# Kernel tuning notes

Measured on AMD Instinct MI355X. Metric: run time of the kernel, lower is better.

The kernel has to match this reference:

```python
import jax, jax.numpy as jnp
import numpy as np

# ---------- static mesh topology helpers (numpy, setup-time only) ----------

def _topo_subdivide(nv, faces):
    edge_id = {}
    mids = []
    nf = []
    def mid(a, b):
        k = (a, b) if a < b else (b, a)
        if k not in edge_id:
            edge_id[k] = nv + len(mids)
            mids.append(k)
        return edge_id[k]
    for a, b, c in faces:
        a, b, c = int(a), int(b), int(c)
        ab, bc, ca = mid(a, b), mid(b, c), mid(c, a)
        nf += [[a, ab, ca], [b, bc, ab], [c, ca, bc], [ab, bc, ca]]
    return np.array(nf, dtype=np.int64), np.array(mids, dtype=np.int64)

def _icosphere(level, radius):
    t = (1.0 + 5.0 ** 0.5) / 2.0
    v = np.array([[-1, t, 0], [1, t, 0], [-1, -t, 0], [1, -t, 0],
                  [0, -1, t], [0, 1, t], [0, -1, -t], [0, 1, -t],
                  [t, 0, -1], [t, 0, 1], [-t, 0, -1], [-t, 0, 1]], dtype=np.float64)
    v /= np.linalg.norm(v, axis=1, keepdims=True)
    f = np.array([[0, 11, 5], [0, 5, 1], [0, 1, 7], [0, 7, 10], [0, 10, 11],
                  [1, 5, 9], [5, 11, 4], [11, 10, 2], [10, 7, 6], [7, 1, 8],
                  [3, 9, 4], [3, 4, 2], [3, 2, 6], [3, 6, 8], [3, 8, 9],
                  [4, 9, 5], [2, 4, 11], [6, 2, 10], [8, 6, 7], [9, 8, 1]], dtype=np.int64)
    for _ in range(level):
        f, mids = _topo_subdivide(len(v), f)
        mv = v[mids[:, 0]] + v[mids[:, 1]]
        mv /= np.linalg.norm(mv, axis=1, keepdims=True)
        v = np.concatenate([v, mv], 0)
    return (v * radius).astype(np.float32), f

def _directed_edges(faces):
    e = np.concatenate([faces[:, [0, 1]], faces[:, [1, 2]], faces[:, [2, 0]],
                        faces[:, [1, 0]], faces[:, [2, 1]], faces[:, [0, 2]]], 0)
    return np.unique(e, axis=0).T.astype(np.int64)  # (2, E) directed, deduped

# ---------- jax forward math ----------

def _project(verts, camera_c, camera_f):
    # K @ [I | t], t = (0,0,0.8): rows [f0,0,c0,0.8*c0],[0,f1,c1,0.8*c1],[0,0,1,0.8]
    z = jnp.zeros((), verts.dtype); o = jnp.ones((), verts.dtype)
    tz = jnp.asarray(0.8, verts.dtype)
    P = jnp.stack([
        jnp.stack([camera_f[0], z, camera_c[0], tz * camera_c[0]]),
        jnp.stack([z, camera_f[1], camera_c[1], tz * camera_c[1]]),
        jnp.stack([z, z, o, tz])])
    hom = jnp.concatenate([verts, jnp.ones((verts.shape[0], 1), verts.dtype)], 1)
    pc = hom @ P.T                     # (V, 3)
    return pc[:, :2] / pc[:, 2:3]      # (V, 2) pixel coords [x, y]

def _bilerp(feat, px, py, image_size):
    # feat: (C, dim, dim); px, py: (V,)
    dim = feat.shape[1]
    x = px * dim / image_size
    y = py * dim / image_size
    x1 = jnp.floor(x); x2 = x1 + 1.0
    y1 = jnp.floor(y); y2 = y1 + 1.0
    xi1 = jnp.clip(x1.astype(jnp.int32), 0, dim - 1)
    xi2 = jnp.clip(x2.astype(jnp.int32), 0, dim - 1)
    yi1 = jnp.clip(y1.astype(jnp.int32), 0, dim - 1)
    yi2 = jnp.clip(y2.astype(jnp.int32), 0, dim - 1)
    f11 = feat[:, xi1, yi1].T  # (V, C)
    f12 = feat[:, xi1, yi2].T
    f21 = feat[:, xi2, yi1].T
    f22 = feat[:, xi2, yi2].T
    w11 = ((x2 - x) * (y2 - y))[:, None]
    w12 = ((x2 - x) * (y - y1))[:, None]
    w21 = ((x - x1) * (y2 - y))[:, None]
    w22 = ((x - x1) * (y - y1))[:, None]
    return w11 * f11 + w12 * f12 + w21 * f21 + w22 * f22

def _gconv(x, W0, W1, b, src, dst):
    agg = jax.ops.segment_sum(x[dst], src, num_segments=x.shape[0])
    return x @ W0 + agg @ W1 + b

def _gresnet(x, edges, params):
    Win0, Win1, bin_, W0s, W1s, bs, Wc0, Wc1, bc = params
    src, dst = edges[0], edges[1]
    h = jax.nn.relu(_gconv(x, Win0, Win1, bin_, src, dst))
    def body(h, lw):
        W0, W1, b = lw
        return jax.nn.relu(_gconv(h, W0, W1, b, src, dst)) + h, None
    h, _ = jax.lax.scan(body, h, (W0s, W1s, bs))
    coords = _gconv(h, Wc0, Wc1, bc, src, dst)
    return h, coords

def _forward(f3, f4, f5, verts0, camera_c, camera_f, p1, p2, p3,
             edges1, edges2, edges3, mid0, mid1, image_size):
    def deform(verts, shape_feat, edges, params):
        pix = _project(verts, camera_c, camera_f)
        px, py = pix[:, 0], pix[:, 1]
        perc = jnp.concatenate([_bilerp(f3, px, py, image_size),
                                _bilerp(f4, px, py, image_size),
                                _bilerp(f5, px, py, image_size)], 1)  # (V, 1280)
        feats = jnp.concatenate([perc, shape_feat], 1)
        h, coords = _gresnet(feats, edges, params)
        return coords, h
    def unpool(verts, feat, mid):
        vf = jnp.concatenate([verts, feat], 1)
        new = (vf[mid[:, 0]] + vf[mid[:, 1]]) * 0.5  # edge midpoints
        vf = jnp.concatenate([vf, new], 0)
        return vf[:, :3], vf[:, 3:]
    verts, feat = deform(verts0, verts0, edges1, p1)
    verts, feat = unpool(verts, feat, mid0)
    verts, feat = deform(verts, feat, edges2, p2)
    verts, feat = unpool(verts, feat, mid1)
    verts, _ = deform(verts, feat, edges3, p3)
    return verts  # (40962, 3)

# ---------- harness entry points ----------

def setup_inputs() -> dict:
    key = jax.random.key(0)
    keys = iter(jax.random.split(key, 64))
    v0, f0 = _icosphere(4, 0.2)                      # 2562 verts, 5120 faces
    f1, mid0 = _topo_subdivide(len(v0), f0)          # -> 10242 verts topology
    f2, mid1 = _topo_subdivide(len(v0) + len(mid0), f1)  # -> 40962 verts
    inp = {
        'f3': jax.random.normal(next(keys), (256, 56, 56), jnp.float32),
        'f4': jax.random.normal(next(keys), (512, 28, 28), jnp.float32),
        'f5': jax.random.normal(next(keys), (512, 14, 14), jnp.float32),
        'verts0': jnp.asarray(v0),
        'camera_c': jnp.array([112.0, 112.0], jnp.float32),
        'camera_f': jnp.array([248.0, 248.0], jnp.float32),
    }
    D, L = 128, 12
    def stage(prefix, in_dim):
        def w(shape, scale):
            return jax.random.normal(next(keys), shape, jnp.float32) * scale
        inp[prefix + '_Win0'] = w((in_dim, D), 1.0 / np.sqrt(in_dim))
        inp[prefix + '_Win1'] = w((in_dim, D), 1.0 / np.sqrt(in_dim))
        inp[prefix + '_bin'] = jnp.zeros((D,), jnp.float32)
        inp[prefix + '_W0'] = w((L, D, D), 0.3 / np.sqrt(D))
        inp[prefix + '_W1'] = w((L, D, D), 0.3 / np.sqrt(D))
        inp[prefix + '_b'] = jnp.zeros((L, D), jnp.float32)
        inp[prefix + '_Wc0'] = w((D, 3), 0.01 / np.sqrt(D))
        inp[prefix + '_Wc1'] = w((D, 3), 0.01 / np.sqrt(D))
        inp[prefix + '_bc'] = jnp.zeros((3,), jnp.float32)
    stage('g1', 1283)
    stage('g2', 1408)
    stage('g3', 1408)
    inp['edges1'] = jnp.asarray(_directed_edges(f0))   # (2, 15360)
    inp['edges2'] = jnp.asarray(_directed_edges(f1))   # (2, 61440)
    inp['edges3'] = jnp.asarray(_directed_edges(f2))   # (2, 245760)
    inp['mid0'] = jnp.asarray(mid0)                    # (7680, 2)
    inp['mid1'] = jnp.asarray(mid1)                    # (30720, 2)
    inp['image_size'] = 224
    return inp

def reference(f3, f4, f5, verts0, camera_c, camera_f,
              g1_Win0, g1_Win1, g1_bin, g1_W0, g1_W1, g1_b, g1_Wc0, g1_Wc1, g1_bc,
              g2_Win0, g2_Win1, g2_bin, g2_W0, g2_W1, g2_b, g2_Wc0, g2_Wc1, g2_bc,
              g3_Win0, g3_Win1, g3_bin, g3_W0, g3_W1, g3_b, g3_Wc0, g3_Wc1, g3_bc,
              edges1, edges2, edges3, mid0, mid1, image_size):
    p1 = (g1_Win0, g1_Win1, g1_bin, g1_W0, g1_W1, g1_b, g1_Wc0, g1_Wc1, g1_bc)
    p2 = (g2_Win0, g2_Win1, g2_bin, g2_W0, g2_W1, g2_b, g2_Wc0, g2_Wc1, g2_bc)
    p3 = (g3_Win0, g3_Win1, g3_bin, g3_W0, g3_W1, g3_b, g3_Wc0, g3_Wc1, g3_bc)
    return _forward(f3, f4, f5, verts0, camera_c, camera_f, p1, p2, p3,
                    edges1, edges2, edges3, mid0, mid1, image_size)
```

## Files before the change

### kernel.cpp

```cpp
#include <hip/hip_runtime.h>
#include <hip/hip_bf16.h>
#include <cstddef>
#include <cstdint>

#define DIV_UP(a, b) (((a) + (b) - 1) / (b))

typedef __attribute__((ext_vector_type(8))) short bf16x8v;
typedef __attribute__((ext_vector_type(4))) float f32x4v;

__device__ __forceinline__ unsigned short bf16_rn(float v) {
    unsigned int u = __float_as_uint(v);
    unsigned int r = (u + 0x7FFFu + ((u >> 16) & 1u)) >> 16;
    return (unsigned short)r;
}
__device__ __forceinline__ float bf16_f(unsigned short h) {
    return __uint_as_float(((unsigned int)h) << 16);
}
__device__ __forceinline__ void f2hl(float v, unsigned short& hi, unsigned short& lo) {
    hi = bf16_rn(v);
    float r = v - bf16_f(hi);
    lo = bf16_rn(r);
}
__device__ __forceinline__ int xcd_swz(int orig, int nwg) {
    int q = nwg >> 3, r = nwg & 7;
    int xcd = orig & 7, idx = orig >> 3;
    return (xcd < r ? xcd * (q + 1) : r * (q + 1) + (xcd - r) * q) + idx;
}

__global__ void transpose_hl(const float* __restrict__ in, unsigned short* __restrict__ ohi,
                             unsigned short* __restrict__ olo, int C, int HW) {
    int idx = blockIdx.x * 256 + threadIdx.x;
    if (idx >= C * HW) return;
    int c = idx % C;
    int p = idx / C;
    float v = in[(size_t)c * HW + p];
    unsigned short hi, lo;
    f2hl(v, hi, lo);
    ohi[(size_t)p * C + c] = hi;
    olo[(size_t)p * C + c] = lo;
}

struct PackArgs {
    const float* Win0[3]; const float* Win1[3];
    const float* W0L[3];  const float* W1L[3];
    unsigned short* BtLp[3];
    unsigned short *BtShi[2], *BtSlo[2];
    unsigned short *Bgh[3], *Bgl[3];
};

__global__ void pack_all(PackArgs p) {
    const int LAY1 = 12 * 32768;
    const int LAYT = 3 * LAY1;
    const int SH1 = 256 * 128;
    const int SHT = 2 * SH1;
    const int GB0 = 768 * 256, GB1 = 768 * 512;
    int idx = blockIdx.x * 256 + threadIdx.x;
    if (idx < LAYT) {
        int st = idx / LAY1, r = idx % LAY1;
        int layer = r >> 15, q = r & 32767;
        int ks = q >> 12, nt = (q >> 9) & 7, lane = (q >> 3) & 63, i = q & 7;
        int n = nt * 16 + (lane & 15);
        int k = ks * 32 + ((lane >> 4) << 3) + i;
        float v = (k < 128) ? p.W0L[st][(size_t)layer * 16384 + k * 128 + n]
                            : p.W1L[st][(size_t)layer * 16384 + (k - 128) * 128 + n];
        unsigned short hi, lo;
        f2hl(v, hi, lo);
        size_t base = ((size_t)layer * 64 + ks * 8 + nt) * 1024 + lane * 8 + i;
        p.BtLp[st][base] = hi;
        p.BtLp[st][base + 512] = lo;
        return;
    }
    float v;
    unsigned short* dh;
    unsigned short* dl;
    size_t o;
    if (idx < LAYT + SHT) {
        int q = idx - LAYT;
        int st = q / SH1, rr = q % SH1;
        int n = rr >> 7, k = rr & 127;
        const float* w0 = p.Win0[st + 1];
        const float* w1 = p.Win1[st + 1];
        v = (n < 128) ? w0[(size_t)(1280 + k) * 128 + n]
                      : w1[(size_t)(1280 + k) * 128 + (n - 128)];
        dh = p.BtShi[st]; dl = p.BtSlo[st]; o = rr;
    } else {
        int q = idx - LAYT - SHT;
        int m, C, base;
        if (q < GB0) { m = 0; C = 256; base = 0; }
        else if (q < GB0 + GB1) { m = 1; C = 512; base = 256; q -= GB0; }
        else if (q < GB0 + 2 * GB1) { m = 2; C = 512; base = 768; q -= GB0 + GB1; }
        else return;
        int n = q / C, k = q % C;
        int s = n >> 8, j = n & 255;
        v = (j < 128) ? p.Win0[s][(size_t)(base + k) * 128 + j]
                      : p.Win1[s][(size_t)(base + k) * 128 + (j - 128)];
        dh = p.Bgh[m]; dl = p.Bgl[m]; o = q;
    }
    unsigned short hi, lo;
    f2hl(v, hi, lo);
    dh[o] = hi;
    dl[o] = lo;
}

__global__ void desc_adj_kernel(const float* __restrict__ verts,
                                const float* __restrict__ cam_c, const float* __restrict__ cam_f,
                                const int* __restrict__ imgsz, int V,
                                const int* __restrict__ src, const int* __restrict__ dst, int E,
                                int* __restrict__ sampi, float* __restrict__ sampw,
                                int* __restrict__ adj8) {
    int v = blockIdx.x * 256 + threadIdx.x;
    if (v >= V) return;
    float X = verts[3 * v + 0], Yy = verts[3 * v + 1], Z = verts[3 * v + 2];
    float cx = cam_c[0], cy = cam_c[1], fx = cam_f[0], fy = cam_f[1];
    const float tz = 0.8f;
    float pz = Z + tz;
    float px = (fx * X + cx * Z + tz * cx) / pz;
    float py = (fy * Yy + cy * Z + tz * cy) / pz;
    float is = (float)imgsz[0];
    const int Ss[3] = {56, 28, 14};
#pragma unroll
    for (int m = 0; m < 3; ++m) {
        int S = Ss[m];
        float dim = (float)S;
        float x = px * dim / is;
        float y = py * dim / is;
        float x1 = floorf(x), y1 = floorf(y);
        float x2 = x1 + 1.0f, y2 = y1 + 1.0f;
        float smax = (float)(S - 1);
        int xi1 = (int)fminf(fmaxf(x1, 0.0f), smax);
        int xi2 = (int)fminf(fmaxf(x2, 0.0f), smax);
        int yi1 = (int)fminf(fmaxf(y1, 0.0f), smax);
        int yi2 = (int)fminf(fmaxf(y2, 0.0f), smax);
        int b = v * 12 + m * 4;
        sampi[b + 0] = xi1 * S + yi1;
        sampi[b + 1] = xi1 * S + yi2;
        sampi[b + 2] = xi2 * S + yi1;
        sampi[b + 3] = xi2 * S + yi2;
        sampw[b + 0] = (x2 - x) * (y2 - y);
        sampw[b + 1] = (x2 - x) * (y - y1);
        sampw[b + 2] = (x - x1) * (y2 - y);
        sampw[b + 3] = (x - x1) * (y - y1);
    }
    int lo = 0, hi = E;
    while (lo < hi) { int m = (lo + hi) >> 1; if (src[m] < v) lo = m + 1; else hi = m; }
    int e0 = lo;
    hi = E;
    while (lo < hi) { int m = (lo + hi) >> 1; if (src[m] < v + 1) lo = m + 1; else hi = m; }
    int e1 = lo;
    int* ap = adj8 + (size_t)v * 8;
#pragma unroll
    for (int i = 0; i < 8; ++i) {
        int e = e0 + i;
        ap[i] = (e < e1) ? dst[e] : -1;
    }
}

struct MArgs {
    const unsigned short *Ahi, *Alo; int lda;
    const unsigned short *Bhi, *Blo; int K;
    float* Y;
    int sstr;
    int V;
};

template <int EPI>
__global__ __launch_bounds__(256) void mgemm(MArgs g) {
    __shared__ unsigned short As_hi[64][40], As_lo[64][40];
    __shared__ unsigned short Bs_hi[128][40], Bs_lo[128][40];
    int tid = threadIdx.x;
    int row0 = blockIdx.y * 64;
    int col0 = blockIdx.x * 128;
    int l = tid & 63, wid = tid >> 6;
    int wr = wid & 1, wc = wid >> 1;
    int lw = l & 15, gg = l >> 4;
    f32x4v acc[2][4];
#pragma unroll
    for (int i = 0; i < 2; ++i)
#pragma unroll
        for (int j = 0; j < 4; ++j) acc[i][j] = (f32x4v){0.f, 0.f, 0.f, 0.f};

    int arow = tid >> 2, akoff = (tid & 3) * 8;
    for (int k0 = 0; k0 < g.K; k0 += 32) {
        __syncthreads();
        {
            int grow = row0 + arow;
            uint4 zh = make_uint4(0, 0, 0, 0), zl = make_uint4(0, 0, 0, 0);
            if (grow < g.V) {
                zh = *(const uint4*)(g.Ahi + (size_t)grow * g.lda + k0 + akoff);
                zl = *(const uint4*)(g.Alo + (size_t)grow * g.lda + k0 + akoff);
            }
            *(uint4*)&As_hi[arow][akoff] = zh;
            *(uint4*)&As_lo[arow][akoff] = zl;
        }
#pragma unroll
        for (int it = 0; it < 2; ++it) {
            int q = tid + it * 256;
            int n = q >> 2, koff = (q & 3) * 8;
            *(uint4*)&Bs_hi[n][koff] = *(const uint4*)(g.Bhi + (size_t)(col0 + n) * g.K + k0 + koff);
            *(uint4*)&Bs_lo[n][koff] = *(const uint4*)(g.Blo + (size_t)(col0 + n) * g.K + k0 + koff);
        }
        __syncthreads();
        bf16x8v ah[2], al[2], bh[4], bl[4];
#pragma unroll
        for (int mt = 0; mt < 2; ++mt) {
            int r = wr * 32 + mt * 16 + lw;
            ah[mt] = *(const bf16x8v*)&As_hi[r][gg * 8];
            al[mt] = *(const bf16x8v*)&As_lo[r][gg * 8];
        }
#pragma unroll
        for (int nt = 0; nt < 4; ++nt) {
            int c = wc * 64 + nt * 16 + lw;
            bh[nt] = *(const bf16x8v*)&Bs_hi[c][gg * 8];
            bl[nt] = *(const bf16x8v*)&Bs_lo[c][gg * 8];
        }
#pragma unroll
        for (int mt = 0; mt < 2; ++mt)
#pragma unroll
            for (int nt = 0; nt < 4; ++nt) {
                acc[mt][nt] = __builtin_amdgcn_mfma_f32_16x16x32_bf16(ah[mt], bh[nt], acc[mt][nt], 0, 0, 0);
                acc[mt][nt] = __builtin_amdgcn_mfma_f32_16x16x32_bf16(ah[mt], bl[nt], acc[mt][nt], 0, 0, 0);
                acc[mt][nt] = __builtin_amdgcn_mfma_f32_16x16x32_bf16(al[mt], bh[nt], acc[mt][nt], 0, 0, 0);
            }
    }
#pragma unroll
    for (int mt = 0; mt < 2; ++mt)
#pragma unroll
        for (int nt = 0; nt < 4; ++nt) {
            int colg = wc * 64 + nt * 16 + lw;
#pragma unroll
            for (int r = 0; r < 4; ++r) {
                int rowg = row0 + wr * 32 + mt * 16 + gg * 4 + r;
                if (rowg >= g.V) continue;
                float v = acc[mt][nt][r];
                if (EPI == 3) {
                    g.Y[(size_t)rowg * 256 + col0 + colg] = v;
                } else {
                    int cg = col0 + colg;
                    g.Y[(size_t)(cg >> 8) * g.sstr + (size_t)rowg * 256 + (cg & 255)] = v;
                }
            }
        }
}

__global__ void gather_kernel(const float* __restrict__ G, int sstr,
                              const int* __restrict__ sampi, const float* __restrict__ sampw,
                              float* __restrict__ Yb, int V, int stage,
                              const float* __restrict__ Win0, const float* __restrict__ Win1,
                              const float* __restrict__ shape) {
    int v = xcd_swz(blockIdx.x, gridDim.x) * 4 + (threadIdx.x >> 6);
    if (v >= V) return;
    int j = (threadIdx.x & 63) * 4;
    const float* Gs = G + (size_t)stage * sstr;
    int b = v * 12;
    float4 acc;
    if (stage == 0) acc = make_float4(0.f, 0.f, 0.f, 0.f);
    else acc = *(const float4*)(Yb + (size_t)v * 256 + j);
#pragma unroll
    for (int s = 0; s < 4; ++s) {
        float w = sampw[b + s];
        float4 f = *(const float4*)(Gs + (size_t)sampi[b + s] * 256 + j);
        acc.x += w * f.x; acc.y += w * f.y; acc.z += w * f.z; acc.w += w * f.w;
    }
#pragma unroll
    for (int s = 0; s < 4; ++s) {
        float w = sampw[b + 4 + s];
        float4 f = *(const float4*)(Gs + (size_t)(3136 + sampi[b + 4 + s]) * 256 + j);
        acc.x += w * f.x; acc.y += w * f.y; acc.z += w * f.z; acc.w += w * f.w;
    }
#pragma unroll
    for (int s = 0; s < 4; ++s) {
        float w = sampw[b + 8 + s];
        float4 f = *(const float4*)(Gs + (size_t)(3920 + sampi[b + 8 + s]) * 256 + j);
        acc.x += w * f.x; acc.y += w * f.y; acc.z += w * f.z; acc.w += w * f.w;
    }
    if (stage == 0) {
#pragma unroll
        for (int k = 0; k < 3; ++k) {
            float w = shape[v * 3 + k];
            const float* wr = (j < 128) ? Win0 + (size_t)(1280 + k) * 128 + j
                                        : Win1 + (size_t)(1280 + k) * 128 + (j - 128);
            float4 wv = *(const float4*)wr;
            acc.x += w * wv.x; acc.y += w * wv.y; acc.z += w * wv.z; acc.w += w * wv.w;
        }
    }
    *(float4*)(Yb + (size_t)v * 256 + j) = acc;
}

__global__ __launch_bounds__(256) void combine_in(
    const float* __restrict__ Y, const float* __restrict__ bias,
    const int* __restrict__ adj8,
    float* __restrict__ hout, int V) {
    int v = xcd_swz(blockIdx.x, gridDim.x) * 8 + (threadIdx.x >> 5);
    if (v >= V) return;
    int d = (threadIdx.x & 31) * 4;
    float4 val = *(const float4*)(Y + (size_t)v * 256 + d);
    float4 b4 = *(const float4*)(bias + d);
    val.x += b4.x; val.y += b4.y; val.z += b4.z; val.w += b4.w;
    const int* ap = adj8 + (size_t)v * 8;
    int n[6];
#pragma unroll
    for (int i = 0; i < 6; ++i) n[i] = ap[i];
#pragma unroll
    for (int i = 0; i < 6; ++i) {
        if (n[i] >= 0) {
            float4 f = *(const float4*)(Y + (size_t)n[i] * 256 + 128 + d);
            val.x += f.x; val.y += f.y; val.z += f.z; val.w += f.w;
        }
    }
    val.x = fmaxf(val.x, 0.f); val.y = fmaxf(val.y, 0.f);
    val.z = fmaxf(val.z, 0.f); val.w = fmaxf(val.w, 0.f);
    *(float4*)(hout + (size_t)v * 128 + d) = val;
}

struct LArgs {
    const float* h;
    const unsigned short* Bp;
    const int* adj8;
    const float* bias;
    float* hnext;
    int V;
};

template <int PAIRS>
__global__ __launch_bounds__(PAIRS * 128) void lay_kernel(LArgs g) {
    __shared__ float psum[PAIRS][16][132];
    int tid = threadIdx.x;
    int wid = tid >> 6, l = tid & 63;
    int pair = wid >> 1, role = wid & 1;
    int rowbase = xcd_swz(blockIdx.x, gridDim.x) * (PAIRS * 16) + pair * 16;
    int lrow = l & 15, lks = l >> 4;
    int grow = rowbase + lrow;
    bool act = grow < g.V;

    f32x4v acc[8];
#pragma unroll
    for (int nt = 0; nt < 8; ++nt) acc[nt] = (f32x4v){0.f, 0.f, 0.f, 0.f};

    if (role == 0) {
        const float* hp = g.h + (size_t)grow * 128;
#pragma unroll
        for (int ks = 0; ks < 4; ++ks) {
            int kb = ks * 32 + lks * 8;
            float a[8];
            if (act) {
                float4 f0 = *(const float4*)(hp + kb);
                float4 f1 = *(const float4*)(hp + kb + 4);
                a[0] = f0.x; a[1] = f0.y; a[2] = f0.z; a[3] = f0.w;
                a[4] = f1.x; a[5] = f1.y; a[6] = f1.z; a[7] = f1.w;
            } else {
#pragma unroll
                for (int i = 0; i < 8; ++i) a[i] = 0.f;
            }
            unsigned short hh[8], ll[8];
#pragma unroll
            for (int i = 0; i < 8; ++i) f2hl(a[i], hh[i], ll[i]);
            bf16x8v ah = *(const bf16x8v*)hh;
            bf16x8v al = *(const bf16x8v*)ll;
#pragma unroll
            for (int nt = 0; nt < 8; ++nt) {
                const unsigned short* p = g.Bp + (size_t)(ks * 8 + nt) * 1024 + l * 8;
                bf16x8v bh = *(const bf16x8v*)p;
                bf16x8v bl = *(const bf16x8v*)(p + 512);
                acc[nt] = __builtin_amdgcn_mfma_f32_16x16x32_bf16(ah, bh, acc[nt], 0, 0, 0);
                acc[nt] = __builtin_amdgcn_mfma_f32_16x16x32_bf16(ah, bl, acc[nt], 0, 0, 0);
                acc[nt] = __builtin_amdgcn_mfma_f32_16x16x32_bf16(al, bh, acc[nt], 0, 0, 0);
            }
        }
    } else {
        int n[6];
        if (act) {
            const int* ap = g.adj8 + (size_t)grow * 8;
#pragma unroll
            for (int i = 0; i < 6; ++i) n[i] = ap[i];
        } else {
#pragma unroll
            for (int i = 0; i < 6; ++i) n[i] = -1;
        }
#pragma unroll
        for (int ks = 0; ks < 4; ++ks) {
            int ko = ks * 32 + lks * 8;
            float a[8];
#pragma unroll
            for (int i = 0; i < 8; ++i) a[i] = 0.f;
#pragma unroll
            for (int i = 0; i < 6; ++i) {
                if (n[i] >= 0) {
                    const float* hp = g.h + (size_t)n[i] * 128 + ko;
                    float4 f0 = *(const float4*)hp;
                    float4 f1 = *(const float4*)(hp + 4);
                    a[0] += f0.x; a[1] += f0.y; a[2] += f0.z; a[3] += f0.w;
                    a[4] += f1.x; a[5] += f1.y; a[6] += f1.z; a[7] += f1.w;
                }
            }
            unsigned short hh[8], ll[8];
#pragma unroll
            for (int i = 0; i < 8; ++i) f2hl(a[i], hh[i], ll[i]);
            bf16x8v ah = *(const bf16x8v*)hh;
            bf16x8v al = *(const bf16x8v*)ll;
#pragma unroll
            for (int nt = 0; nt < 8; ++nt) {
                const unsigned short* p = g.Bp + (size_t)((ks + 4) * 8 + nt) * 1024 + l * 8;
                bf16x8v bh = *(const bf16x8v*)p;
                bf16x8v bl = *(const bf16x8v*)(p + 512);
                acc[nt] = __builtin_amdgcn_mfma_f32_16x16x32_bf16(ah, bh, acc[nt], 0, 0, 0);
                acc[nt] = __builtin_amdgcn_mfma_f32_16x16x32_bf16(ah, bl, acc[nt], 0, 0, 0);
                acc[nt] = __builtin_amdgcn_mfma_f32_16x16x32_bf16(al, bh, acc[nt], 0, 0, 0);
            }
        }
#pragma unroll
        for (int nt = 0; nt < 8; ++nt)
#pragma unroll
            for (int r = 0; r < 4; ++r)
                psum[pair][lks * 4 + r][nt * 16 + lrow] = acc[nt][r];
    }
    __syncthreads();
    if (role == 0) {
#pragma unroll
        for (int nt = 0; nt < 8; ++nt) {
            int colg = nt * 16 + lrow;
            float bv = g.bias[colg];
#pragma unroll
            for (int r = 0; r < 4; ++r) {
                int rowg = rowbase + lks * 4 + r;
                if (rowg < g.V) {
                    float v = acc[nt][r] + psum[pair][lks * 4 + r][colg] + bv;
                    v = fmaxf(v, 0.0f);
                    v += g.h[(size_t)rowg * 128 + colg];
                    g.hnext[(size_t)rowg * 128 + colg] = v;
                }
            }
        }
    }
}

__global__ void coordgemm_kernel(const float* __restrict__ h,
                                 const float* __restrict__ Wc0, const float* __restrict__ Wc1,
                                 int V, float* __restrict__ Yc) {
    int idx = blockIdx.x * 256 + threadIdx.x;
    if (idx >= V * 6) return;
    int v = idx / 6, j = idx % 6;
    const float* W = (j < 3) ? Wc0 : Wc1;
    int jj = (j < 3) ? j : j - 3;
    const float* hp = h + (size_t)v * 128;
    float acc = 0.0f;
#pragma unroll
    for (int k = 0; k < 32; ++k) {
        float4 f = *(const float4*)(hp + k * 4);
        acc += f.x * W[(k * 4 + 0) * 3 + jj];
        acc += f.y * W[(k * 4 + 1) * 3 + jj];
        acc += f.z * W[(k * 4 + 2) * 3 + jj];
        acc += f.w * W[(k * 4 + 3) * 3 + jj];
    }
    Yc[idx] = acc;
}

__global__ void coordcombine_kernel(const float* __restrict__ Yc, const float* __restrict__ bc,
                                    const int* __restrict__ adj8,
                                    int V, float* __restrict__ out) {
    int idx = blockIdx.x * 256 + threadIdx.x;
    if (idx >= V * 3) return;
    int v = idx / 3, j = idx % 3;
    float val = Yc[(size_t)v * 6 + j] + bc[j];
    const int* ap = adj8 + (size_t)v * 8;
    int n[6];
#pragma unroll
    for (int i = 0; i < 6; ++i) n[i] = ap[i];
#pragma unroll
    for (int i = 0; i < 6; ++i)
        if (n[i] >= 0) val += Yc[(size_t)n[i] * 6 + 3 + j];
    out[(size_t)v * 3 + j] = val;
}

__global__ void unpool_kernel(float* __restrict__ verts, const float* __restrict__ h,
                              const int* __restrict__ mid, int V, int Nm,
                              unsigned short* __restrict__ fphi, unsigned short* __restrict__ fplo) {
    int r = blockIdx.x;
    int t = threadIdx.x;
    if (r < V) {
        float v = h[(size_t)r * 128 + t];
        unsigned short hi, lo;
        f2hl(v, hi, lo);
        fphi[(size_t)r * 128 + t] = hi;
        fplo[(size_t)r * 128 + t] = lo;
    } else {
        int i = r - V;
        int a = mid[2 * i], b = mid[2 * i + 1];
        float v = 0.5f * (h[(size_t)a * 128 + t] + h[(size_t)b * 128 + t]);
        unsigned short hi, lo;
        f2hl(v, hi, lo);
        fphi[(size_t)r * 128 + t] = hi;
        fplo[(size_t)r * 128 + t] = lo;
        if (t < 3)
            verts[(size_t)r * 3 + t] = 0.5f * (verts[(size_t)a * 3 + t] + verts[(size_t)b * 3 + t]);
    }
}

extern "C" void kernel_launch(void* const* d_in, const int* in_sizes, int n_in,
                              void* d_out, int out_size, void* d_ws, size_t ws_size,
                              hipStream_t stream) {
    const float* f3 = (const float*)d_in[0];
    const float* f4 = (const float*)d_in[1];
    const float* f5 = (const float*)d_in[2];
    const float* verts0 = (const float*)d_in[3];
    const float* cam_c = (const float*)d_in[4];
    const float* cam_f = (const float*)d_in[5];
    const int* imgsz = (const int*)d_in[38];

    int V0 = in_sizes[3] / 3;
    int E[3] = {in_sizes[33] / 2, in_sizes[34] / 2, in_sizes[35] / 2};
    int Nm0 = in_sizes[36] / 2, Nm1 = in_sizes[37] / 2;
    int V1 = V0 + Nm0, V2 = V1 + Nm1;
    int Vs[3] = {V0, V1, V2};
    const int NPIXT = 3136 + 784 + 196;
    const int GS = NPIXT * 256;

    char* wsp = (char*)d_ws;
    auto alloc = [&](size_t bytes) -> void* {
        void* p = (void*)wsp;
        wsp += (bytes + 255) & ~(size_t)255;
        return p;
    };
    unsigned short* ft0h = (unsigned short*)alloc((size_t)3136 * 256 * 2);
    unsigned short* ft0l = (unsigned short*)alloc((size_t)3136 * 256 * 2);
    unsigned short* ft1h = (unsigned short*)alloc((size_t)784 * 512 * 2);
    unsigned short* ft1l = (unsigned short*)alloc((size_t)784 * 512 * 2);
    unsigned short* ft2h = (unsigned short*)alloc((size_t)196 * 512 * 2);
    unsigned short* ft2l = (unsigned short*)alloc((size_t)196 * 512 * 2);
    unsigned short* Bg0h = (unsigned short*)alloc((size_t)768 * 256 * 2);
    unsigned short* Bg0l = (unsigned short*)alloc((size_t)768 * 256 * 2);
    unsigned short* Bg1h = (unsigned short*)alloc((size_t)768 * 512 * 2);
    unsigned short* Bg1l = (unsigned short*)alloc((size_t)768 * 512 * 2);
    unsigned short* Bg2h = (unsigned short*)alloc((size_t)768 * 512 * 2);
    unsigned short* Bg2l = (unsigned short*)alloc((size_t)768 * 512 * 2);
    float* Gbuf = (float*)alloc((size_t)3 * GS * 4);
    unsigned short* BtLp[3];
    for (int s = 0; s < 3; ++s)
        BtLp[s] = (unsigned short*)alloc((size_t)12 * 65536 * 2);
    unsigned short* BtShi[2];
    unsigned short* BtSlo[2];
    for (int s = 0; s < 2; ++s) {
        BtShi[s] = (unsigned short*)alloc((size_t)256 * 128 * 2);
        BtSlo[s] = (unsigned short*)alloc((size_t)256 * 128 * 2);
    }
    float* Ybuf = (float*)alloc((size_t)V2 * 256 * 4);
    float* hA = (float*)alloc((size_t)V2 * 128 * 4);
    float* hB = (float*)alloc((size_t)V2 * 128 * 4);
    unsigned short* FPhi = (unsigned short*)alloc((size_t)V2 * 128 * 2);
    unsigned short* FPlo = (unsigned short*)alloc((size_t)V2 * 128 * 2);
    float* vertsbuf = (float*)alloc((size_t)V2 * 3 * 4);
    float* Yc = (float*)alloc((size_t)V2 * 6 * 4);
    int* sampi = (int*)alloc((size_t)V2 * 12 * 4);
    float* sampw = (float*)alloc((size_t)V2 * 12 * 4);
    int* adj8 = (int*)alloc((size_t)V2 * 8 * 4);

    transpose_hl<<<DIV_UP(256 * 56 * 56, 256), 256, 0, stream>>>(f3, ft0h, ft0l, 256, 56 * 56);
    transpose_hl<<<DIV_UP(512 * 28 * 28, 256), 256, 0, stream>>>(f4, ft1h, ft1l, 512, 28 * 28);
    transpose_hl<<<DIV_UP(512 * 14 * 14, 256), 256, 0, stream>>>(f5, ft2h, ft2l, 512, 14 * 14);

    {
        PackArgs p;
        for (int s = 0; s < 3; ++s) {
            p.Win0[s] = (const float*)d_in[6 + s * 9 + 0];
            p.Win1[s] = (const float*)d_in[6 + s * 9 + 1];
            p.W0L[s] = (const float*)d_in[6 + s * 9 + 3];
            p.W1L[s] = (const float*)d_in[6 + s * 9 + 4];
            p.BtLp[s] = BtLp[s];
        }
        p.BtShi[0] = BtShi[0]; p.BtSlo[0] = BtSlo[0];
        p.BtShi[1] = BtShi[1]; p.BtSlo[1] = BtSlo[1];
        p.Bgh[0] = Bg0h; p.Bgl[0] = Bg0l;
        p.Bgh[1] = Bg1h; p.Bgl[1] = Bg1l;
        p.Bgh[2] = Bg2h; p.Bgl[2] = Bg2l;
        int total = 3 * 12 * 32768 + 2 * 256 * 128 + 768 * 256 + 2 * 768 * 512;
        pack_all<<<DIV_UP(total, 256), 256, 0, stream>>>(p);
    }

    {
        MArgs m = {};
        m.sstr = GS;
        m.Ahi = ft0h; m.Alo = ft0l; m.lda = 256;
        m.Bhi = Bg0h; m.Blo = Bg0l; m.K = 256;
        m.Y = Gbuf; m.V = 3136;
        dim3 g0(6, DIV_UP(3136, 64));
        mgemm<2><<<g0, 256, 0, stream>>>(m);
        m.Ahi = ft1h; m.Alo = ft1l; m.lda = 512;
        m.Bhi = Bg1h; m.Blo = Bg1l; m.K = 512;
        m.Y = Gbuf + (size_t)3136 * 256; m.V = 784;
        dim3 g1(6, DIV_UP(784, 64));
        mgemm<2><<<g1, 256, 0, stream>>>(m);
        m.Ahi = ft2h; m.Alo = ft2l; m.lda = 512;
        m.Bhi = Bg2h; m.Blo = Bg2l; m.K = 512;
        m.Y = Gbuf + (size_t)3920 * 256; m.V = 196;
        dim3 g2(6, DIV_UP(196, 64));
        mgemm<2><<<g2, 256, 0, stream>>>(m);
    }

    for (int si = 0; si < 3; ++si) {
        const float* Win0 = (const float*)d_in[6 + si * 9 + 0];
        const float* Win1 = (const float*)d_in[6 + si * 9 + 1];
        const float* bin = (const float*)d_in[6 + si * 9 + 2];
        const float* bs = (const float*)d_in[6 + si * 9 + 5];
        const float* Wc0 = (const float*)d_in[6 + si * 9 + 6];
        const float* Wc1 = (const float*)d_in[6 + si * 9 + 7];
        const float* bc = (const float*)d_in[6 + si * 9 + 8];
        const int* edges = (const int*)d_in[33 + si];
        int Ecur = E[si];
        const int* esrc = edges;
        const int* edst = edges + Ecur;
        int V = Vs[si];
        const float* vertsin = (si == 0) ? verts0 : vertsbuf;

        desc_adj_kernel<<<DIV_UP(V, 256), 256, 0, stream>>>(vertsin, cam_c, cam_f, imgsz, V,
                                                            esrc, edst, Ecur, sampi, sampw, adj8);
        if (si > 0) {
            MArgs m = {};
            m.Ahi = FPhi; m.Alo = FPlo; m.lda = 128;
            m.Bhi = BtShi[si - 1]; m.Blo = BtSlo[si - 1]; m.K = 128;
            m.Y = Ybuf; m.V = V;
            dim3 grid(2, DIV_UP(V, 64));
            mgemm<3><<<grid, 256, 0, stream>>>(m);
        }
        gather_kernel<<<DIV_UP(V, 4), 256, 0, stream>>>(Gbuf, GS, sampi, sampw, Ybuf, V, si,
                                                        Win0, Win1, (si == 0) ? verts0 : nullptr);
        combine_in<<<DIV_UP(V, 8), 256, 0, stream>>>(Ybuf, bin, adj8, hA, V);

        float* hcur = hA;
        float* hnext = hB;
        for (int ll = 0; ll < 12; ++ll) {
            LArgs a = {};
            a.h = hcur;
            a.Bp = BtLp[si] + (size_t)ll * 65536;
            a.adj8 = adj8;
            a.bias = bs + (size_t)ll * 128;
            a.hnext = hnext;
            a.V = V;
            if (si == 2) {
                lay_kernel<2><<<DIV_UP(V, 32), 256, 0, stream>>>(a);
            } else {
                lay_kernel<1><<<DIV_UP(V, 16), 128, 0, stream>>>(a);
            }
            float* t = hcur; hcur = hnext; hnext = t;
        }

        coordgemm_kernel<<<DIV_UP(V * 6, 256), 256, 0, stream>>>(hcur, Wc0, Wc1, V, Yc);
        float* ctarget = (si == 2) ? (float*)d_out : vertsbuf;
        coordcombine_kernel<<<DIV_UP(V * 3, 256), 256, 0, stream>>>(Yc, bc, adj8, V, ctarget);
        if (si < 2) {
            const int* mid = (const int*)d_in[36 + si];
            int Nm = (si == 0) ? Nm0 : Nm1;
            unpool_kernel<<<V + Nm, 128, 0, stream>>>(vertsbuf, hcur, mid, V, Nm, FPhi, FPlo);
        }
    }
}
```

Baseline: 1.409 ms.

## Split graph-conv layer kernel across four waves by K and N halves per 16 rows

The layer kernel now uses four waves per 16-row tile, splitting both the reduction (self vs neighbour-sum halves) and the output columns (two halves of 128). Each wave holds 4 accumulator tiles instead of 8, and the epilogue is rewritten so every thread does vectorized float4 bias/ReLU/residual writes from two shared-memory partial buffers. The goal is more parallelism and occupancy for small meshes and coalesced stores. The cost is duplicated A-operand loads and neighbour gathers across the N-split waves, plus a shared-memory round trip for all partials.

```diff
diff --git a/kernel.cpp b/kernel.cpp
--- a/kernel.cpp
+++ b/kernel.cpp
@@ -321,22 +321,22 @@
     int V;
 };
 
-template <int PAIRS>
-__global__ __launch_bounds__(PAIRS * 128) void lay_kernel(LArgs g) {
-    __shared__ float psum[PAIRS][16][132];
+__global__ __launch_bounds__(256, 4) void lay_kernel(LArgs g) {
+    __shared__ float psA[16][132];
+    __shared__ float psB[16][132];
     int tid = threadIdx.x;
     int wid = tid >> 6, l = tid & 63;
-    int pair = wid >> 1, role = wid & 1;
-    int rowbase = xcd_swz(blockIdx.x, gridDim.x) * (PAIRS * 16) + pair * 16;
+    int role_k = wid & 1, role_n = wid >> 1;
+    int rowbase = xcd_swz(blockIdx.x, gridDim.x) * 16;
     int lrow = l & 15, lks = l >> 4;
     int grow = rowbase + lrow;
     bool act = grow < g.V;
 
-    f32x4v acc[8];
-#pragma unroll
-    for (int nt = 0; nt < 8; ++nt) acc[nt] = (f32x4v){0.f, 0.f, 0.f, 0.f};
-
-    if (role == 0) {
+    f32x4v acc[4];
+#pragma unroll
+    for (int nt = 0; nt < 4; ++nt) acc[nt] = (f32x4v){0.f, 0.f, 0.f, 0.f};
+
+    if (role_k == 0) {
         const float* hp = g.h + (size_t)grow * 128;
 #pragma unroll
         for (int ks = 0; ks < 4; ++ks) {
@@ -357,8 +357,9 @@
             bf16x8v ah = *(const bf16x8v*)hh;
             bf16x8v al = *(const bf16x8v*)ll;
 #pragma unroll
-            for (int nt = 0; nt < 8; ++nt) {
-                const unsigned short* p = g.Bp + (size_t)(ks * 8 + nt) * 1024 + l * 8;
+            for (int nt = 0; nt < 4; ++nt) {
+                int ntg = role_n * 4 + nt;
+                const unsigned short* p = g.Bp + (size_t)(ks * 8 + ntg) * 1024 + l * 8;
                 bf16x8v bh = *(const bf16x8v*)p;
                 bf16x8v bl = *(const bf16x8v*)(p + 512);
                 acc[nt] = __builtin_amdgcn_mfma_f32_16x16x32_bf16(ah, bh, acc[nt], 0, 0, 0);
@@ -398,8 +399,9 @@
             bf16x8v ah = *(const bf16x8v*)hh;
             bf16x8v al = *(const bf16x8v*)ll;
 #pragma unroll
-            for (int nt = 0; nt < 8; ++nt) {
-                const unsigned short* p = g.Bp + (size_t)((ks + 4) * 8 + nt) * 1024 + l * 8;
+            for (int nt = 0; nt < 4; ++nt) {
+                int ntg = role_n * 4 + nt;
+                const unsigned short* p = g.Bp + (size_t)((ks + 4) * 8 + ntg) * 1024 + l * 8;
                 bf16x8v bh = *(const bf16x8v*)p;
                 bf16x8v bl = *(const bf16x8v*)(p + 512);
                 acc[nt] = __builtin_amdgcn_mfma_f32_16x16x32_bf16(ah, bh, acc[nt], 0, 0, 0);
@@ -407,28 +409,37 @@
                 acc[nt] = __builtin_amdgcn_mfma_f32_16x16x32_bf16(al, bh, acc[nt], 0, 0, 0);
             }
         }
-#pragma unroll
-        for (int nt = 0; nt < 8; ++nt)
-#pragma unroll
-            for (int r = 0; r < 4; ++r)
-                psum[pair][lks * 4 + r][nt * 16 + lrow] = acc[nt][r];
+    }
+
+    {
+        float(*ps)[132] = role_k ? psA : psB;
+#pragma unroll
+        for (int nt = 0; nt < 4; ++nt) {
+            int col = role_n * 64 + nt * 16 + lrow;
+#pragma unroll
+            for (int r = 0; r < 4; ++r) ps[lks * 4 + r][col] = acc[nt][r];
+        }
     }
     __syncthreads();
-    if (role == 0) {
-#pragma unroll
-        for (int nt = 0; nt < 8; ++nt) {
-            int colg = nt * 16 + lrow;
-            float bv = g.bias[colg];
-#pragma unroll
-            for (int r = 0; r < 4; ++r) {
-                int rowg = rowbase + lks * 4 + r;
-                if (rowg < g.V) {
-                    float v = acc[nt][r] + psum[pair][lks * 4 + r][colg] + bv;
-                    v = fmaxf(v, 0.0f);
-                    v += g.h[(size_t)rowg * 128 + colg];
-                    g.hnext[(size_t)rowg * 128 + colg] = v;
-                }
-            }
+
+    int erow = tid >> 5;
+    int ecol = (tid & 31) * 4;
+    float4 b4 = *(const float4*)(g.bias + ecol);
+#pragma unroll
+    for (int rr = 0; rr < 2; ++rr) {
+        int row = rr * 8 + erow;
+        int rowg = rowbase + row;
+        if (rowg < g.V) {
+            float4 s;
+            s.x = psA[row][ecol + 0] + psB[row][ecol + 0] + b4.x;
+            s.y = psA[row][ecol + 1] + psB[row][ecol + 1] + b4.y;
+            s.z = psA[row][ecol + 2] + psB[row][ecol + 2] + b4.z;
+            s.w = psA[row][ecol + 3] + psB[row][ecol + 3] + b4.w;
+            s.x = fmaxf(s.x, 0.f); s.y = fmaxf(s.y, 0.f);
+            s.z = fmaxf(s.z, 0.f); s.w = fmaxf(s.w, 0.f);
+            float4 hres = *(const float4*)(g.h + (size_t)rowg * 128 + ecol);
+            s.x += hres.x; s.y += hres.y; s.z += hres.z; s.w += hres.w;
+            *(float4*)(g.hnext + (size_t)rowg * 128 + ecol) = s;
         }
     }
 }
@@ -634,11 +645,7 @@
             a.bias = bs + (size_t)ll * 128;
             a.hnext = hnext;
             a.V = V;
-            if (si == 2) {
-                lay_kernel<2><<<DIV_UP(V, 32), 256, 0, stream>>>(a);
-            } else {
-                lay_kernel<1><<<DIV_UP(V, 16), 128, 0, stream>>>(a);
-            }
+            lay_kernel<<<DIV_UP(V, 16), 256, 0, stream>>>(a);
             float* t = hcur; hcur = hnext; hnext = t;
         }
 
```

Result: no change. 1.385 ms (-1.8%).
